# Performance work log

Hardware: AMD Instinct MI355X
Metric: run time of the kernel (lower is better)

The kernel has to match this reference:

```python
import jax, jax.numpy as jnp
import numpy as np

HEADS = 8
GS = 16
C = 512
E = 512
SCALE = (E / HEADS) ** -0.5
PNAMES = ['sa_qkv_w','sa_qkv_b','sa_pa_w','sa_pa_b','sa_ln1_g','sa_ln1_b','sa_f1_w','sa_f1_b','sa_f2_w','sa_f2_b','sa_ln2_g','sa_ln2_b','sa_c1_w','sa_c1_b','sa_c2_w','sa_c2_b','sa_bn_g','sa_bn_b','ca_q_w','ca_q_b','ca_k_w','ca_k_b','ca_v_w','ca_v_b','ca_pa_w','ca_pa_b','p_q_w','p_q_b','p_k_w','p_k_b','p_v_w','p_v_b','p_pa_w','p_pa_b','p_ln_g','p_ln_b','p_lin_w','p_lin_b']


def _ln(x, g, b, eps=1e-5):
    m = x.mean(-1, keepdims=True)
    v = jnp.var(x, axis=-1, keepdims=True)
    return (x - m) / jnp.sqrt(v + eps) * g + b


def _conv1x1(x, w, b):
    return jnp.einsum('bchw,oc->bohw', x, w) + b[None, :, None, None]


def _up_ac(x, out=GS):
    # bilinear upsample, align_corners=True (nn.UpsamplingBilinear2d)
    H = x.shape[2]
    pos = jnp.arange(out) * (H - 1) / (out - 1)
    lo = jnp.floor(pos).astype(jnp.int32)
    hi = jnp.minimum(lo + 1, H - 1)
    w = (pos - lo).astype(x.dtype)
    xr = x[:, :, lo, :] * (1 - w)[None, None, :, None] + x[:, :, hi, :] * w[None, None, :, None]
    return xr[:, :, :, lo] * (1 - w) + xr[:, :, :, hi] * w


def _asri(x, p):
    # Sequence_ASRI: GAP tokens -> attention over the batch axis -> pixel-shuffle back
    B = x.shape[0]; ch = E // HEADS
    gap = x.mean((2, 3))                                             # [B,C]
    qkv = (gap @ p['sa_qkv_w'].T + p['sa_qkv_b']).reshape(B, 4, ch, HEADS).transpose(1, 3, 0, 2)  # [4,H,B,ch]
    q, k, v, skip = qkv[0], qkv[1], qkv[2], qkv[3]
    attn = jax.nn.softmax(jnp.einsum('hbc,hdc->hbd', q, k) * SCALE, -1)  # [H,B,B]
    o = jnp.einsum('hbd,hdc->hbc', attn, v)
    merge = lambda t: t.transpose(1, 2, 0).reshape(B, E)             # 'head b c -> b (c head)'
    a = merge(o) @ p['sa_pa_w'].T + p['sa_pa_b'] + merge(skip)
    h = jax.nn.relu(_ln(a, p['sa_ln1_g'], p['sa_ln1_b']) @ p['sa_f1_w'].T + p['sa_f1_b'])
    a = h @ p['sa_f2_w'].T + p['sa_f2_b'] + a
    s = _ln(a, p['sa_ln2_g'], p['sa_ln2_b']) @ p['sa_c1_w'].T + p['sa_c1_b']  # [B,C*16]
    s = _up_ac(s.reshape(B, C, 4, 4))                                 # pixel shuffle p1=p2=4 then bilinear to 16x16
    s = _conv1x1(s, p['sa_c2_w'], p['sa_c2_b'])
    # BatchNorm2d in eval mode (running_mean=0, running_var=1, eps=1e-5)
    s = s / np.float32(np.sqrt(1.0 + 1e-5)) * p['sa_bn_g'][None, :, None, None] + p['sa_bn_b'][None, :, None, None]
    return x + jax.nn.relu(s)


def _sscm(x1, x2, p):
    # Sequence_SSCM: GAP-token q/k over batch axis, full spatial v
    B = x1.shape[0]; ch = E // HEADS
    q = (x1.mean((2, 3)) @ p['ca_q_w'].T + p['ca_q_b']).reshape(B, ch, HEADS).transpose(2, 0, 1)  # [H,B,ch]
    k = (x2.mean((2, 3)) @ p['ca_k_w'].T + p['ca_k_b']).reshape(B, ch, HEADS).transpose(2, 0, 1)
    v = _conv1x1(x2, p['ca_v_w'], p['ca_v_b']).reshape(B, ch, HEADS, GS, GS).transpose(2, 0, 1, 3, 4).reshape(HEADS, B, ch * GS * GS)
    attn = jax.nn.softmax(jnp.einsum('hbc,hdc->hbd', q, k) * SCALE, -1)  # [H,B,B]
    o = jnp.einsum('hbd,hdm->hbm', attn, v)
    o = o.reshape(HEADS, B, ch, GS, GS).transpose(1, 2, 0, 3, 4).reshape(B, E, GS, GS)
    return jax.nn.relu(_conv1x1(o, p['ca_pa_w'], p['ca_pa_b']))


def _pixel(x1, x2, p):
    # Pixel_SSCM: pixel-wise cross-batch attention (no scale -- matches source)
    B = x1.shape[0]; ch = E // HEADS; N = GS * GS
    split = lambda t: t.reshape(B, ch, HEADS, N).transpose(2, 0, 3, 1)   # 'b (c head) h w -> head b (h w) c'
    q = split(_conv1x1(x1, p['p_q_w'], p['p_q_b']))                      # [H,B,N,ch]
    k = split(_conv1x1(x2, p['p_k_w'], p['p_k_b']))
    v = split(_conv1x1(x2, p['p_v_w'], p['p_v_b'])).reshape(HEADS, B * N, ch)
    attn = jax.nn.softmax(jnp.einsum('hbnc,hqmc->hbqnm', q, k), -1)      # [H,B,B,N,N]
    attn = attn.transpose(1, 0, 3, 2, 4).reshape(B, HEADS, N, B * N)     # 'head b q h w -> b head h (q w)'
    o = jnp.einsum('bhnm,hmc->bhnc', attn, v)
    o = o.transpose(0, 3, 1, 2).reshape(B, E, GS, GS)                    # 'b head (h w) c -> b (c head) h w'
    o = _conv1x1(o, p['p_pa_w'], p['p_pa_b']) + x1
    t = o.reshape(B, C, N).transpose(0, 2, 1)                            # [B,N,C]
    t = jax.nn.relu(_ln(t, p['p_ln_g'], p['p_ln_b']) @ p['p_lin_w'].T + p['p_lin_b'])
    return t.transpose(0, 2, 1).reshape(B, C, GS, GS)


def _hrlm(p, xs, xq):
    sa_s = _asri(xs, p)
    sa_q = _asri(xq, p)
    ca_s = _sscm(sa_s, sa_q, p)
    ca_q = _sscm(sa_q, sa_s, p)
    return _pixel(sa_s, ca_q, p), _pixel(sa_q, ca_s, p)


def setup_inputs():
    key = jax.random.key(0)
    ks = iter(jax.random.split(key, 64))
    w = lambda *s: (jax.random.normal(next(ks), s) * 0.02).astype(jnp.float32)
    z = lambda n: jnp.zeros((n,), jnp.float32)
    o = lambda n: jnp.ones((n,), jnp.float32)
    return dict(
        fea_support=jax.random.normal(next(ks), (8, C, GS, GS), jnp.float32),
        fea_query=jax.random.normal(next(ks), (8, C, GS, GS), jnp.float32),
        sa_qkv_w=w(4 * E, C), sa_qkv_b=z(4 * E),
        sa_pa_w=w(E, E), sa_pa_b=z(E),
        sa_ln1_g=o(E), sa_ln1_b=z(E),
        sa_f1_w=w(E, E), sa_f1_b=z(E), sa_f2_w=w(E, E), sa_f2_b=z(E),
        sa_ln2_g=o(E), sa_ln2_b=z(E),
        sa_c1_w=w(C * 16, E), sa_c1_b=z(C * 16),
        sa_c2_w=w(C, E), sa_c2_b=z(C),
        sa_bn_g=o(C), sa_bn_b=z(C),
        ca_q_w=w(E, C), ca_q_b=z(E), ca_k_w=w(E, C), ca_k_b=z(E),
        ca_v_w=w(E, C), ca_v_b=z(E), ca_pa_w=w(C, E), ca_pa_b=z(C),
        p_q_w=w(E, C), p_q_b=z(E), p_k_w=w(E, C), p_k_b=z(E),
        p_v_w=w(E, C), p_v_b=z(E), p_pa_w=w(C, E), p_pa_b=z(C),
        p_ln_g=o(C), p_ln_b=z(C), p_lin_w=w(C, C), p_lin_b=z(C),
    )


def reference(fea_support, fea_query, sa_qkv_w, sa_qkv_b, sa_pa_w, sa_pa_b, sa_ln1_g, sa_ln1_b, sa_f1_w, sa_f1_b, sa_f2_w, sa_f2_b, sa_ln2_g, sa_ln2_b, sa_c1_w, sa_c1_b, sa_c2_w, sa_c2_b, sa_bn_g, sa_bn_b, ca_q_w, ca_q_b, ca_k_w, ca_k_b, ca_v_w, ca_v_b, ca_pa_w, ca_pa_b, p_q_w, p_q_b, p_k_w, p_k_b, p_v_w, p_v_b, p_pa_w, p_pa_b, p_ln_g, p_ln_b, p_lin_w, p_lin_b):
    p = dict(zip(PNAMES, (sa_qkv_w, sa_qkv_b, sa_pa_w, sa_pa_b, sa_ln1_g, sa_ln1_b, sa_f1_w, sa_f1_b, sa_f2_w, sa_f2_b, sa_ln2_g, sa_ln2_b, sa_c1_w, sa_c1_b, sa_c2_w, sa_c2_b, sa_bn_g, sa_bn_b, ca_q_w, ca_q_b, ca_k_w, ca_k_b, ca_v_w, ca_v_b, ca_pa_w, ca_pa_b, p_q_w, p_q_b, p_k_w, p_k_b, p_v_w, p_v_b, p_pa_w, p_pa_b, p_ln_g, p_ln_b, p_lin_w, p_lin_b)))
    return _hrlm(p, fea_support, fea_query)
```

## Files before the change

### kernel.cpp

```cpp
#include <hip/hip_runtime.h>
#include <cmath>

#define IMG 131072
#define BIGF 1048576

#define CF_RELU  1
#define CF_RES   2
#define CF_BN    4
#define CF_SPLIT 8
#define CF_TRANS 16

typedef __attribute__((ext_vector_type(8))) short short8;
typedef __attribute__((ext_vector_type(4))) short short4v;
typedef __attribute__((ext_vector_type(4))) float f32x4;

__device__ __forceinline__ float wave_sum(float v){
    #pragma unroll
    for (int off = 32; off; off >>= 1) v += __shfl_xor(v, off);
    return v;
}

__device__ __forceinline__ unsigned short bf16_rn(float x){
    union { float f; unsigned u; } v; v.f = x;
    unsigned r = v.u + 0x7FFF + ((v.u >> 16) & 1);
    return (unsigned short)(r >> 16);
}
__device__ __forceinline__ float bf16_to_f(unsigned short h){
    union { float f; unsigned u; } v; v.u = ((unsigned)h) << 16;
    return v.f;
}
__device__ __forceinline__ unsigned pk_hi(unsigned a, unsigned b){
    return __builtin_amdgcn_perm(b, a, 0x05040100u);
}
__device__ __forceinline__ unsigned pk_lo(unsigned a, unsigned b){
    return __builtin_amdgcn_perm(b, a, 0x07060302u);
}

struct GapJobs  { const float* x[2]; float* o[2]; };
struct G8Job    { const float* in; const float* W; const float* bias; const float* add; float* out; };
struct G8Jobs   { G8Job j[4]; };
struct AAJobs   { const float* qkv[2]; float* om[2]; };
struct LnJobs   { const float* in[2]; float* out[2]; };
struct UpJobs   { const float* in[2]; float* out[2]; };
struct SAJobs   { const float* q8[2]; const float* k8[2]; float* aw[2]; };
struct SPJobs   { const float* aw[2]; const float* v[2]; float* out[2]; };
struct ZJobs    { float* p[2]; };
struct ConvJob  { const float* X; const float* W; const float* B; const float* R;
                  const float* bng; const float* bnb; float* O; int flags; };
struct ConvJobs { ConvJob j[6]; };
struct PixJob   { const unsigned* Q; const unsigned* K; const unsigned* V; float* O; };
struct PixJobs  { PixJob j[2]; };

__global__ __launch_bounds__(64) void k_gap(GapJobs jo){
    const int br = blockIdx.y;
    const int bc = blockIdx.x;
    const int lane = threadIdx.x;
    const float* p = jo.x[br] + (size_t)bc * 256;
    float s = p[lane] + p[lane + 64] + p[lane + 128] + p[lane + 192];
    s = wave_sum(s);
    if (lane == 0) jo.o[br][bc] = s * (1.0f / 256.0f);
}

__global__ __launch_bounds__(64) void k_gemm8(G8Jobs jo, int add_off, int add_stride, int O, int relu){
    const G8Job j = jo.j[blockIdx.y];
    const int o = blockIdx.x;
    const int lane = threadIdx.x;
    const float* wr = j.W + (size_t)o * 512;
    float acc[8] = {0,0,0,0,0,0,0,0};
    #pragma unroll
    for (int i = 0; i < 8; i++){
        float w = wr[lane + 64*i];
        #pragma unroll
        for (int b = 0; b < 8; b++) acc[b] += w * j.in[b*512 + lane + 64*i];
    }
    #pragma unroll
    for (int b = 0; b < 8; b++) acc[b] = wave_sum(acc[b]);
    if (lane < 8){
        float v = acc[0];
        #pragma unroll
        for (int b = 1; b < 8; b++) if (lane == b) v = acc[b];
        v += j.bias[o];
        if (j.add) v += j.add[lane*add_stride + add_off + o];
        if (relu) v = fmaxf(v, 0.f);
        j.out[(size_t)lane * O + o] = v;
    }
}

__global__ __launch_bounds__(64) void k_asri_attn(AAJobs jo){
    const int br = blockIdx.y;
    const float* qkv = jo.qkv[br];
    const int h = blockIdx.x >> 3, b = blockIdx.x & 7, c = threadIdx.x;
    const int ci = c*8 + h;
    float qc = qkv[b*2048 + ci];
    float s[8];
    #pragma unroll
    for (int d = 0; d < 8; d++){
        float p = qc * qkv[d*2048 + 512 + ci];
        p = wave_sum(p);
        s[d] = p * 0.125f;
    }
    float m = s[0];
    #pragma unroll
    for (int d = 1; d < 8; d++) m = fmaxf(m, s[d]);
    float sum = 0.f;
    #pragma unroll
    for (int d = 0; d < 8; d++){ s[d] = __expf(s[d]-m); sum += s[d]; }
    float r = 1.f / sum;
    float oc = 0.f;
    #pragma unroll
    for (int d = 0; d < 8; d++) oc += s[d]*r * qkv[d*2048 + 1024 + ci];
    jo.om[br][b*512 + ci] = oc;
}

__global__ __launch_bounds__(64) void k_ln8(LnJobs jo,
    const float* __restrict__ g, const float* __restrict__ be)
{
    const int br = blockIdx.y;
    const int b = blockIdx.x, lane = threadIdx.x;
    const float* in = jo.in[br];
    float v[8]; float s = 0.f;
    #pragma unroll
    for (int i = 0; i < 8; i++){ v[i] = in[b*512 + lane + 64*i]; s += v[i]; }
    s = wave_sum(s);
    float mean = s * (1.f/512.f);
    float q = 0.f;
    #pragma unroll
    for (int i = 0; i < 8; i++){ float d = v[i]-mean; q += d*d; }
    q = wave_sum(q);
    float rstd = rsqrtf(q*(1.f/512.f) + 1e-5f);
    #pragma unroll
    for (int i = 0; i < 8; i++){
        int c = lane + 64*i;
        jo.out[br][b*512 + c] = (v[i]-mean)*rstd*g[c] + be[c];
    }
}

__global__ __launch_bounds__(256) void k_up(UpJobs jo){
    const int br = blockIdx.y;
    const int idx = blockIdx.x*256 + threadIdx.x;
    const int x = idx & 15, y = (idx >> 4) & 15, bc = idx >> 8;
    float px = (float)(x*3) / 15.0f, py = (float)(y*3) / 15.0f;
    int lx = (int)px, ly = (int)py;
    float wx = px - lx, wy = py - ly;
    int hx = min(lx+1, 3), hy = min(ly+1, 3);
    const float* p = jo.in[br] + (size_t)bc * 16;
    float v00 = p[ly*4+lx], v01 = p[ly*4+hx], v10 = p[hy*4+lx], v11 = p[hy*4+hx];
    float a0 = v00*(1.f-wy) + v10*wy;
    float a1 = v01*(1.f-wy) + v11*wy;
    jo.out[br][idx] = a0*(1.f-wx) + a1*wx;
}

__global__ __launch_bounds__(256) void k_zero(ZJobs jo){
    jo.p[blockIdx.y][(size_t)blockIdx.x*256 + threadIdx.x] = 0.f;
}

#define LDK 40
__device__ __forceinline__ void convm_body(
    const float* __restrict__ Xb, const float* __restrict__ W,
    const float* __restrict__ bias, const float* __restrict__ resb,
    const float* __restrict__ bng, const float* __restrict__ bnb, float bninv,
    float* __restrict__ outb, int flags, int o0, int n0, unsigned short* lds)
{
    const int tid512 = threadIdx.x;
    const int g   = tid512 >> 8;
    const int tid = tid512 & 255;
    unsigned short* sAh = lds + g*10240;
    unsigned short* sAl = sAh + 2560;
    unsigned short* sBh = sAl + 2560;
    unsigned short* sBl = sBh + 2560;
    const int wv = tid >> 6, lane = tid & 63;
    const int quad = lane >> 4, l16 = lane & 15;
    const int wo = (wv >> 1) * 32, wn = (wv & 1) * 32;
    const int so  = tid >> 2, sk8 = (tid & 3) * 8;
    const int sp  = tid & 15, sn  = (tid >> 4) * 4;

    const float* wrow = W + (size_t)(o0 + so)*512 + g*256 + sk8;
    const float* xrow = Xb + (size_t)(g*256 + 2*sp)*256 + n0 + sn;

    f32x4 acc[2][2] = {};
    float4 a0 = *(const float4*)(wrow);
    float4 a1 = *(const float4*)(wrow + 4);
    float4 x0 = *(const float4*)(xrow);
    float4 x1 = *(const float4*)(xrow + 256);

    for (int k0 = 0; k0 < 256; k0 += 32){
        __syncthreads();
        {
            float wa[8] = {a0.x,a0.y,a0.z,a0.w,a1.x,a1.y,a1.z,a1.w};
            #pragma unroll
            for (int j = 0; j < 4; j++){
                unsigned short h0 = bf16_rn(wa[2*j]);
                unsigned short h1 = bf16_rn(wa[2*j+1]);
                unsigned short g0 = bf16_rn(wa[2*j]   - bf16_to_f(h0));
                unsigned short g1 = bf16_rn(wa[2*j+1] - bf16_to_f(h1));
                *(unsigned*)&sAh[so*LDK + sk8 + 2*j] = (unsigned)h0 | ((unsigned)h1 << 16);
                *(unsigned*)&sAl[so*LDK + sk8 + 2*j] = (unsigned)g0 | ((unsigned)g1 << 16);
            }
            float xe[4] = {x0.x,x0.y,x0.z,x0.w};
            float xo[4] = {x1.x,x1.y,x1.z,x1.w};
            #pragma unroll
            for (int j = 0; j < 4; j++){
                unsigned short h0 = bf16_rn(xe[j]);
                unsigned short h1 = bf16_rn(xo[j]);
                unsigned short g0 = bf16_rn(xe[j] - bf16_to_f(h0));
                unsigned short g1 = bf16_rn(xo[j] - bf16_to_f(h1));
                *(unsigned*)&sBh[(sn+j)*LDK + 2*sp] = (unsigned)h0 | ((unsigned)h1 << 16);
                *(unsigned*)&sBl[(sn+j)*LDK + 2*sp] = (unsigned)g0 | ((unsigned)g1 << 16);
            }
        }
        __syncthreads();
        if (k0 + 32 < 256){
            a0 = *(const float4*)(wrow + k0 + 32);
            a1 = *(const float4*)(wrow + k0 + 36);
            x0 = *(const float4*)(xrow + (size_t)(k0+32)*256);
            x1 = *(const float4*)(xrow + (size_t)(k0+32)*256 + 256);
        }
        short8 ah[2], al[2], bh[2], bl[2];
        #pragma unroll
        for (int t = 0; t < 2; t++){
            int ai = (wo + 16*t + l16)*LDK + quad*8;
            ah[t] = *(const short8*)&sAh[ai];
            al[t] = *(const short8*)&sAl[ai];
            int bi = (wn + 16*t + l16)*LDK + quad*8;
            bh[t] = *(const short8*)&sBh[bi];
            bl[t] = *(const short8*)&sBl[bi];
        }
        #pragma unroll
        for (int mt = 0; mt < 2; mt++){
            #pragma unroll
            for (int nt = 0; nt < 2; nt++){
                acc[mt][nt] = __builtin_amdgcn_mfma_f32_16x16x32_bf16(ah[mt], bh[nt], acc[mt][nt], 0, 0, 0);
                acc[mt][nt] = __builtin_amdgcn_mfma_f32_16x16x32_bf16(ah[mt], bl[nt], acc[mt][nt], 0, 0, 0);
                acc[mt][nt] = __builtin_amdgcn_mfma_f32_16x16x32_bf16(al[mt], bh[nt], acc[mt][nt], 0, 0, 0);
            }
        }
    }
    __syncthreads();
    float* red = (float*)lds;
    if (g == 1){
        float* r = red + tid*20;
        #pragma unroll
        for (int mt = 0; mt < 2; mt++)
            #pragma unroll
            for (int nt = 0; nt < 2; nt++)
                *(f32x4*)(r + (mt*2+nt)*4) = acc[mt][nt];
    }
    __syncthreads();
    if (g == 0){
        float* r = red + tid*20;
        #pragma unroll
        for (int mt = 0; mt < 2; mt++)
            #pragma unroll
            for (int nt = 0; nt < 2; nt++){
                f32x4 o4 = *(const f32x4*)(r + (mt*2+nt)*4);
                acc[mt][nt] += o4;
            }
        #pragma unroll
        for (int mt = 0; mt < 2; mt++){
            #pragma unroll
            for (int nt = 0; nt < 2; nt++){
                const int n  = n0 + wn + 16*nt + l16;
                const int ob = o0 + wo + 16*mt + quad*4;
                #pragma unroll
                for (int rr = 0; rr < 4; rr++){
                    const int o = ob + rr;
                    float v = acc[mt][nt][rr] + bias[o];
                    if (flags & CF_BN)   v = v*(bninv*bng[o]) + bnb[o];
                    if (flags & CF_RELU) v = fmaxf(v, 0.f);
                    if (flags & CF_RES)  v += resb[(size_t)o*256 + n];
                    if (flags & CF_SPLIT){
                        unsigned short hi = bf16_rn(v);
                        unsigned short lo = bf16_rn(v - bf16_to_f(hi));
                        unsigned pk = (unsigned)hi | ((unsigned)lo << 16);
                        unsigned* op = (unsigned*)outb;
                        if (flags & CF_TRANS) op[(size_t)n*512 + (o&7)*64 + (o>>3)] = pk;
                        else                  op[(size_t)o*256 + n] = pk;
                    } else {
                        outb[(size_t)o*256 + n] = v;
                    }
                }
            }
        }
    }
}

__global__ __launch_bounds__(512) void k_convm(ConvJobs jo, float bninv)
{
    __shared__ unsigned short lds[20480];
    const int z = blockIdx.z;
    const ConvJob j = jo.j[z >> 3];
    const int b = z & 7;
    convm_body(j.X + (size_t)b*IMG, j.W, j.B, j.R ? j.R + (size_t)b*IMG : nullptr,
               j.bng, j.bnb, bninv, j.O + (size_t)b*IMG, j.flags,
               blockIdx.y*64, blockIdx.x*64, lds);
}

__global__ __launch_bounds__(64) void k_sscm_attn(SAJobs jo)
{
    const int br = blockIdx.y;
    const int h = blockIdx.x >> 3, b = blockIdx.x & 7, c = threadIdx.x;
    const int ci = c*8 + h;
    float qc = jo.q8[br][b*512 + ci];
    float s[8];
    #pragma unroll
    for (int d = 0; d < 8; d++){
        float p = qc * jo.k8[br][d*512 + ci];
        p = wave_sum(p);
        s[d] = p * 0.125f;
    }
    float m = s[0];
    #pragma unroll
    for (int d = 1; d < 8; d++) m = fmaxf(m, s[d]);
    float sum = 0.f;
    #pragma unroll
    for (int d = 0; d < 8; d++){ s[d] = __expf(s[d]-m); sum += s[d]; }
    float r = 1.f/sum;
    if (c < 8){
        float v = s[0];
        #pragma unroll
        for (int d = 1; d < 8; d++) if (c == d) v = s[d];
        jo.aw[br][blockIdx.x*8 + c] = v*r;
    }
}

__global__ __launch_bounds__(256) void k_sscm_apply(SPJobs jo)
{
    const int br = blockIdx.y;
    const int idx = blockIdx.x*256 + threadIdx.x;
    const int pix = idx & 255, e = (idx >> 8) & 511, b = idx >> 17;
    const int h = e & 7;
    const float* aw = jo.aw[br] + (h*8 + b)*8;
    const float* v = jo.v[br];
    float acc = 0.f;
    #pragma unroll
    for (int d = 0; d < 8; d++) acc += aw[d] * v[(size_t)d*IMG + (size_t)e*256 + pix];
    jo.out[br][idx] = acc;
}

__global__ __launch_bounds__(256) void k_pixel_mfma(PixJobs jo)
{
    __shared__ char smem[61440];
    unsigned short* sQh = (unsigned short*)smem;
    unsigned short* sQl = sQh + 2*64*40;
    unsigned short* sKh = sQl + 2*64*40;
    unsigned short* sKl = sKh + 2*128*40;
    unsigned short* sP  = (unsigned short*)smem;
    unsigned short* sVh = sP  + 4*64*40;
    unsigned short* sVl = sVh + 4*64*40;

    const int br = blockIdx.y >> 3, b = blockIdx.y & 7;
    const PixJob J = jo.j[br];
    const int nt = blockIdx.x & 3, d = blockIdx.x >> 2;
    const int h = blockIdx.z;
    const int tid = threadIdx.x;
    const int wv = tid >> 6, lane = tid & 63;
    const int quad = lane >> 4, l16 = lane & 15;
    const int n0 = nt * 64;

    {
        const unsigned* Qt = J.Q + (size_t)b*IMG + (size_t)n0*512 + h*64;
        const int q = tid >> 2, i0 = (tid & 3) * 16;
        const unsigned* src = Qt + (size_t)q*512 + i0;
        uint4 w0 = *(const uint4*)(src);
        uint4 w1 = *(const uint4*)(src + 4);
        uint4 w2 = *(const uint4*)(src + 8);
        uint4 w3 = *(const uint4*)(src + 12);
        unsigned hb[8], lb[8];
        hb[0]=pk_hi(w0.x,w0.y); hb[1]=pk_hi(w0.z,w0.w); hb[2]=pk_hi(w1.x,w1.y); hb[3]=pk_hi(w1.z,w1.w);
        hb[4]=pk_hi(w2.x,w2.y); hb[5]=pk_hi(w2.z,w2.w); hb[6]=pk_hi(w3.x,w3.y); hb[7]=pk_hi(w3.z,w3.w);
        lb[0]=pk_lo(w0.x,w0.y); lb[1]=pk_lo(w0.z,w0.w); lb[2]=pk_lo(w1.x,w1.y); lb[3]=pk_lo(w1.z,w1.w);
        lb[4]=pk_lo(w2.x,w2.y); lb[5]=pk_lo(w2.z,w2.w); lb[6]=pk_lo(w3.x,w3.y); lb[7]=pk_lo(w3.z,w3.w);
        int dst = (i0>>5)*2560 + q*40 + (i0&31);
        *(uint4*)&sQh[dst]     = *(uint4*)&hb[0];
        *(uint4*)&sQh[dst + 8] = *(uint4*)&hb[4];
        *(uint4*)&sQl[dst]     = *(uint4*)&lb[0];
        *(uint4*)&sQl[dst + 8] = *(uint4*)&lb[4];
    }
    __syncthreads();

    short8 bqh[2], bql[2];
    #pragma unroll
    for (int ks = 0; ks < 2; ks++){
        int idx = ks*2560 + (wv*16 + l16)*40 + quad*8;
        bqh[ks] = *(const short8*)&sQh[idx];
        bql[ks] = *(const short8*)&sQl[idx];
    }

    f32x4 S[16] = {};
    #pragma unroll
    for (int hm = 0; hm < 2; hm++){
        __syncthreads();
        {
            const unsigned* Kt = J.K + (size_t)d*IMG + (size_t)hm*128*512 + h*64;
            const int mloc = tid & 127, cb0 = tid >> 7;
            #pragma unroll
            for (int p = 0; p < 4; p++){
                int cb = cb0 + 2*p;
                const unsigned* src = Kt + (size_t)mloc*512 + cb*8;
                uint4 wa = *(const uint4*)(src);
                uint4 wb = *(const uint4*)(src + 4);
                union { short8 s; unsigned u[4]; } hu, lu;
                hu.u[0]=pk_hi(wa.x,wa.y); hu.u[1]=pk_hi(wa.z,wa.w);
                hu.u[2]=pk_hi(wb.x,wb.y); hu.u[3]=pk_hi(wb.z,wb.w);
                lu.u[0]=pk_lo(wa.x,wa.y); lu.u[1]=pk_lo(wa.z,wa.w);
                lu.u[2]=pk_lo(wb.x,wb.y); lu.u[3]=pk_lo(wb.z,wb.w);
                int idx = (cb>>2)*5120 + mloc*40 + (cb&3)*8;
                *(short8*)&sKh[idx] = hu.s;
                *(short8*)&sKl[idx] = lu.s;
            }
        }
        __syncthreads();
        #pragma unroll
        for (int mtl = 0; mtl < 8; mtl++){
            #pragma unroll
            for (int ks = 0; ks < 2; ks++){
                int idx = ks*5120 + (mtl*16 + l16)*40 + quad*8;
                short8 ah = *(const short8*)&sKh[idx];
                short8 al = *(const short8*)&sKl[idx];
                S[hm*8+mtl] = __builtin_amdgcn_mfma_f32_16x16x32_bf16(ah, bqh[ks], S[hm*8+mtl], 0, 0, 0);
                S[hm*8+mtl] = __builtin_amdgcn_mfma_f32_16x16x32_bf16(ah, bql[ks], S[hm*8+mtl], 0, 0, 0);
                S[hm*8+mtl] = __builtin_amdgcn_mfma_f32_16x16x32_bf16(al, bqh[ks], S[hm*8+mtl], 0, 0, 0);
            }
        }
    }

    {
        float mx = -3.4e38f;
        #pragma unroll
        for (int t = 0; t < 16; t++)
            #pragma unroll
            for (int r = 0; r < 4; r++) mx = fmaxf(mx, S[t][r]);
        mx = fmaxf(mx, __shfl_xor(mx, 16));
        mx = fmaxf(mx, __shfl_xor(mx, 32));
        float sum = 0.f;
        #pragma unroll
        for (int t = 0; t < 16; t++)
            #pragma unroll
            for (int r = 0; r < 4; r++){ S[t][r] = __expf(S[t][r]-mx); sum += S[t][r]; }
        sum += __shfl_xor(sum, 16);
        sum += __shfl_xor(sum, 32);
        float rr = 1.f/sum;
        #pragma unroll
        for (int t = 0; t < 16; t++)
            #pragma unroll
            for (int r = 0; r < 4; r++) S[t][r] *= rr;
    }

    f32x4 oac[4] = {};
    #pragma unroll
    for (int hm = 0; hm < 2; hm++){
        __syncthreads();
        #pragma unroll
        for (int mtl = 0; mtl < 8; mtl++){
            short4v p4;
            #pragma unroll
            for (int r = 0; r < 4; r++) p4[r] = (short)bf16_rn(S[hm*8+mtl][r]);
            int idx = (mtl>>1)*2560 + (wv*16 + l16)*40 + 16*(mtl&1) + quad*4;
            *(short4v*)&sP[idx] = p4;
        }
        {
            const unsigned* Vp = J.V + (size_t)d*IMG + (size_t)h*256 + hm*128;
            const int mp = tid & 63, c0 = tid >> 6;
            #pragma unroll
            for (int p = 0; p < 16; p++){
                int c = c0 + 4*p;
                const unsigned* src = Vp + (size_t)c*2048 + 2*mp;
                uint2 w = *(const uint2*)(src);
                int idx = (mp>>4)*2560 + c*40 + ((2*mp)&31);
                *(unsigned*)&sVh[idx] = pk_hi(w.x, w.y);
                *(unsigned*)&sVl[idx] = pk_lo(w.x, w.y);
            }
        }
        __syncthreads();
        #pragma unroll
        for (int ks = 0; ks < 4; ks++){
            int pidx = ks*2560 + (wv*16 + l16)*40 + quad*8;
            short8 bp = *(const short8*)&sP[pidx];
            #pragma unroll
            for (int ct = 0; ct < 4; ct++){
                int vidx = ks*2560 + (ct*16 + l16)*40 + quad*8;
                short8 vh = *(const short8*)&sVh[vidx];
                short8 vl = *(const short8*)&sVl[vidx];
                oac[ct] = __builtin_amdgcn_mfma_f32_16x16x32_bf16(vh, bp, oac[ct], 0, 0, 0);
                oac[ct] = __builtin_amdgcn_mfma_f32_16x16x32_bf16(vl, bp, oac[ct], 0, 0, 0);
            }
        }
    }

    {
        float* Ob = J.O + (size_t)b * IMG;
        const int q = n0 + wv*16 + l16;
        #pragma unroll
        for (int ct = 0; ct < 4; ct++){
            #pragma unroll
            for (int r = 0; r < 4; r++){
                int c = ct*16 + quad*4 + r;
                unsafeAtomicAdd(&Ob[(size_t)(c*8+h)*256 + q], oac[ct][r]);
            }
        }
    }
}

__global__ __launch_bounds__(64) void k_ln_pix(LnJobs jo,
    const float* __restrict__ g, const float* __restrict__ be)
{
    const int br = blockIdx.y;
    const int bn = blockIdx.x;
    const int b = bn >> 8, n = bn & 255;
    const int lane = threadIdx.x;
    const float* p = jo.in[br] + (size_t)b*IMG + n;
    float v[8]; float s = 0.f;
    #pragma unroll
    for (int i = 0; i < 8; i++){ v[i] = p[(size_t)(lane + 64*i)*256]; s += v[i]; }
    s = wave_sum(s);
    float mean = s * (1.f/512.f);
    float q = 0.f;
    #pragma unroll
    for (int i = 0; i < 8; i++){ float d = v[i]-mean; q += d*d; }
    q = wave_sum(q);
    float rstd = rsqrtf(q*(1.f/512.f) + 1e-5f);
    #pragma unroll
    for (int i = 0; i < 8; i++){
        int c = lane + 64*i;
        jo.out[br][(size_t)b*IMG + (size_t)c*256 + n] = (v[i]-mean)*rstd*g[c] + be[c];
    }
}

extern "C" void kernel_launch(void* const* d_in, const int* in_sizes, int n_in,
                              void* d_out, int out_size, void* d_ws, size_t ws_size,
                              hipStream_t stream)
{
    const float* xs    = (const float*)d_in[0];
    const float* xq    = (const float*)d_in[1];
    const float* qkvw  = (const float*)d_in[2];  const float* qkvb = (const float*)d_in[3];
    const float* paw   = (const float*)d_in[4];  const float* pab  = (const float*)d_in[5];
    const float* ln1g  = (const float*)d_in[6];  const float* ln1b = (const float*)d_in[7];
    const float* f1w   = (const float*)d_in[8];  const float* f1b  = (const float*)d_in[9];
    const float* f2w   = (const float*)d_in[10]; const float* f2b  = (const float*)d_in[11];
    const float* ln2g  = (const float*)d_in[12]; const float* ln2b = (const float*)d_in[13];
    const float* c1w   = (const float*)d_in[14]; const float* c1b  = (const float*)d_in[15];
    const float* c2w   = (const float*)d_in[16]; const float* c2b  = (const float*)d_in[17];
    const float* bng   = (const float*)d_in[18]; const float* bnb  = (const float*)d_in[19];
    const float* caqw  = (const float*)d_in[20]; const float* caqb = (const float*)d_in[21];
    const float* cakw  = (const float*)d_in[22]; const float* cakb = (const float*)d_in[23];
    const float* cavw  = (const float*)d_in[24]; const float* cavb = (const float*)d_in[25];
    const float* capw  = (const float*)d_in[26]; const float* capb = (const float*)d_in[27];
    const float* pqw   = (const float*)d_in[28]; const float* pqb  = (const float*)d_in[29];
    const float* pkw   = (const float*)d_in[30]; const float* pkb  = (const float*)d_in[31];
    const float* pvw   = (const float*)d_in[32]; const float* pvb  = (const float*)d_in[33];
    const float* ppw   = (const float*)d_in[34]; const float* ppb  = (const float*)d_in[35];
    const float* plng  = (const float*)d_in[36]; const float* plnb = (const float*)d_in[37];
    const float* plinw = (const float*)d_in[38]; const float* plinb= (const float*)d_in[39];

    const size_t SMF = 262144;
    float* ws = (float*)d_ws;
    float* smb = ws;
    float* B[12];
    for (int i = 0; i < 12; i++) B[i] = ws + SMF + (size_t)i*BIGF;
    float* sa_s = B[0]; float* sa_q = B[1];
    float* ca_s = B[2]; float* ca_q = B[3];
    const bool paired_pixel = ws_size >= (SMF + 12*(size_t)BIGF)*sizeof(float) + 1024;

    auto SM = [&](int br){ return smb + (size_t)br*131072; };
    auto GAP=[&](int br){ return SM(br); };            auto QKV=[&](int br){ return SM(br)+4096; };
    auto OM =[&](int br){ return SM(br)+20480; };      auto AA =[&](int br){ return SM(br)+24576; };
    auto HB =[&](int br){ return SM(br)+28672; };      auto A2 =[&](int br){ return SM(br)+32768; };
    auto LNB=[&](int br){ return SM(br)+36864; };      auto S8 =[&](int br){ return SM(br)+40960; };
    auto ATW=[&](int br){ return SM(br)+106496; };     auto Q8 =[&](int br){ return SM(br)+107008; };
    auto K8 =[&](int br){ return SM(br)+111104; };

    const float bninv = 1.0f / sqrtf(1.0f + 1e-5f);
    float* out0 = (float*)d_out;
    float* out1 = out0 + (size_t)BIGF;

    {
        GapJobs gj = {{xs, xq}, {GAP(0), GAP(1)}};
        k_gap<<<dim3(4096,2), 64, 0, stream>>>(gj);
        G8Jobs qj = {{{GAP(0), qkvw, qkvb, nullptr, QKV(0)}, {GAP(1), qkvw, qkvb, nullptr, QKV(1)}}};
        k_gemm8<<<dim3(2048,2), 64, 0, stream>>>(qj, 0, 0, 2048, 0);
        AAJobs aj = {{QKV(0), QKV(1)}, {OM(0), OM(1)}};
        k_asri_attn<<<dim3(64,2), 64, 0, stream>>>(aj);
        G8Jobs pj = {{{OM(0), paw, pab, QKV(0), AA(0)}, {OM(1), paw, pab, QKV(1), AA(1)}}};
        k_gemm8<<<dim3(512,2), 64, 0, stream>>>(pj, 1536, 2048, 512, 0);
        LnJobs l1 = {{AA(0), AA(1)}, {LNB(0), LNB(1)}};
        k_ln8<<<dim3(8,2), 64, 0, stream>>>(l1, ln1g, ln1b);
        G8Jobs fj = {{{LNB(0), f1w, f1b, nullptr, HB(0)}, {LNB(1), f1w, f1b, nullptr, HB(1)}}};
        k_gemm8<<<dim3(512,2), 64, 0, stream>>>(fj, 0, 0, 512, 1);
        G8Jobs f2j = {{{HB(0), f2w, f2b, AA(0), A2(0)}, {HB(1), f2w, f2b, AA(1), A2(1)}}};
        k_gemm8<<<dim3(512,2), 64, 0, stream>>>(f2j, 0, 512, 512, 0);
        LnJobs l2 = {{A2(0), A2(1)}, {LNB(0), LNB(1)}};
        k_ln8<<<dim3(8,2), 64, 0, stream>>>(l2, ln2g, ln2b);
        G8Jobs cj = {{{LNB(0), c1w, c1b, nullptr, S8(0)}, {LNB(1), c1w, c1b, nullptr, S8(1)}}};
        k_gemm8<<<dim3(8192,2), 64, 0, stream>>>(cj, 0, 0, 8192, 0);
        UpJobs uj = {{S8(0), S8(1)}, {B[4], B[5]}};
        k_up<<<dim3(4096,2), 256, 0, stream>>>(uj);
        ConvJobs c2j = {};
        c2j.j[0] = {B[4], c2w, c2b, xs, bng, bnb, sa_s, CF_BN|CF_RELU|CF_RES};
        c2j.j[1] = {B[5], c2w, c2b, xq, bng, bnb, sa_q, CF_BN|CF_RELU|CF_RES};
        k_convm<<<dim3(4,8,16), 512, 0, stream>>>(c2j, bninv);
    }

    {
        GapJobs gj = {{sa_s, sa_q}, {GAP(0), GAP(1)}};
        k_gap<<<dim3(4096,2), 64, 0, stream>>>(gj);
        G8Jobs qj = {{{GAP(0), caqw, caqb, nullptr, Q8(0)},
                      {GAP(1), cakw, cakb, nullptr, K8(0)},
                      {GAP(1), caqw, caqb, nullptr, Q8(1)},
                      {GAP(0), cakw, cakb, nullptr, K8(1)}}};
        k_gemm8<<<dim3(512,4), 64, 0, stream>>>(qj, 0, 0, 512, 0);
        SAJobs sj = {{Q8(0), Q8(1)}, {K8(0), K8(1)}, {ATW(0), ATW(1)}};
        k_sscm_attn<<<dim3(64,2), 64, 0, stream>>>(sj);
        ConvJobs vj = {};
        vj.j[0] = {sa_q, cavw, cavb, nullptr, nullptr, nullptr, B[4], 0};
        vj.j[1] = {sa_s, cavw, cavb, nullptr, nullptr, nullptr, B[5], 0};
        k_convm<<<dim3(4,8,16), 512, 0, stream>>>(vj, 1.f);
        SPJobs pj = {{ATW(0), ATW(1)}, {B[4], B[5]}, {B[6], B[7]}};
        k_sscm_apply<<<dim3(4096,2), 256, 0, stream>>>(pj);
        ConvJobs aj = {};
        aj.j[0] = {B[6], capw, capb, nullptr, nullptr, nullptr, ca_s, CF_RELU};
        aj.j[1] = {B[7], capw, capb, nullptr, nullptr, nullptr, ca_q, CF_RELU};
        k_convm<<<dim3(4,8,16), 512, 0, stream>>>(aj, 1.f);
    }

    if (paired_pixel){
        ConvJobs qkvj = {};
        qkvj.j[0] = {sa_s, pqw, pqb, nullptr, nullptr, nullptr, B[4],  CF_SPLIT|CF_TRANS};
        qkvj.j[1] = {ca_q, pkw, pkb, nullptr, nullptr, nullptr, B[5],  CF_SPLIT|CF_TRANS};
        qkvj.j[2] = {ca_q, pvw, pvb, nullptr, nullptr, nullptr, B[6],  CF_SPLIT};
        qkvj.j[3] = {sa_q, pqw, pqb, nullptr, nullptr, nullptr, B[8],  CF_SPLIT|CF_TRANS};
        qkvj.j[4] = {ca_s, pkw, pkb, nullptr, nullptr, nullptr, B[9],  CF_SPLIT|CF_TRANS};
        qkvj.j[5] = {ca_s, pvw, pvb, nullptr, nullptr, nullptr, B[10], CF_SPLIT};
        k_convm<<<dim3(4,8,48), 512, 0, stream>>>(qkvj, 1.f);
        ZJobs zj = {{B[7], B[11]}};
        k_zero<<<dim3(4096,2), 256, 0, stream>>>(zj);
        PixJobs pxj = {{{(const unsigned*)B[4], (const unsigned*)B[5], (const unsigned*)B[6], B[7]},
                        {(const unsigned*)B[8], (const unsigned*)B[9], (const unsigned*)B[10], B[11]}}};
        k_pixel_mfma<<<dim3(32,16,8), 256, 0, stream>>>(pxj);
        ConvJobs ppj = {};
        ppj.j[0] = {B[7],  ppw, ppb, sa_s, nullptr, nullptr, out0, CF_RES};
        ppj.j[1] = {B[11], ppw, ppb, sa_q, nullptr, nullptr, out1, CF_RES};
        k_convm<<<dim3(4,8,16), 512, 0, stream>>>(ppj, 1.f);
        LnJobs lj = {{out0, out1}, {B[4], B[8]}};
        k_ln_pix<<<dim3(2048,2), 64, 0, stream>>>(lj, plng, plnb);
        ConvJobs lnj = {};
        lnj.j[0] = {B[4], plinw, plinb, nullptr, nullptr, nullptr, out0, CF_RELU};
        lnj.j[1] = {B[8], plinw, plinb, nullptr, nullptr, nullptr, out1, CF_RELU};
        k_convm<<<dim3(4,8,16), 512, 0, stream>>>(lnj, 1.f);
    } else {
        auto pixel1 = [&](const float* x1, const float* x2, float* out){
            ConvJobs qkvj = {};
            qkvj.j[0] = {x1, pqw, pqb, nullptr, nullptr, nullptr, B[4], CF_SPLIT|CF_TRANS};
            qkvj.j[1] = {x2, pkw, pkb, nullptr, nullptr, nullptr, B[5], CF_SPLIT|CF_TRANS};
            qkvj.j[2] = {x2, pvw, pvb, nullptr, nullptr, nullptr, B[6], CF_SPLIT};
            k_convm<<<dim3(4,8,24), 512, 0, stream>>>(qkvj, 1.f);
            ZJobs zj = {{B[7], B[7]}};
            k_zero<<<dim3(4096,1), 256, 0, stream>>>(zj);
            PixJobs pxj = {{{(const unsigned*)B[4], (const unsigned*)B[5], (const unsigned*)B[6], B[7]},
                            {(const unsigned*)B[4], (const unsigned*)B[5], (const unsigned*)B[6], B[7]}}};
            k_pixel_mfma<<<dim3(32,8,8), 256, 0, stream>>>(pxj);
            ConvJobs ppj = {};
            ppj.j[0] = {B[7], ppw, ppb, x1, nullptr, nullptr, out, CF_RES};
            k_convm<<<dim3(4,8,8), 512, 0, stream>>>(ppj, 1.f);
            LnJobs lj = {{out, out}, {B[4], B[4]}};
            k_ln_pix<<<dim3(2048,1), 64, 0, stream>>>(lj, plng, plnb);
            ConvJobs lnj = {};
            lnj.j[0] = {B[4], plinw, plinb, nullptr, nullptr, nullptr, out, CF_RELU};
            k_convm<<<dim3(4,8,8), 512, 0, stream>>>(lnj, 1.f);
        };
        pixel1(sa_s, ca_q, out0);
        pixel1(sa_q, ca_s, out1);
    }

    (void)in_sizes; (void)n_in; (void)out_size;
}
```

Measured before the change: 492.6 us.

## Shrink pixel-attention LDS footprint and coalesce transposed split conv output

The pixel attention kernel now stages K and V in smaller 64-row chunks over more loop iterations, cutting shared memory per block from 60KB to 40KB so more blocks can be resident per CU. The cost is extra barriers and a finer load/compute interleave. Separately, the conv kernel's transposed split-output path permutes the weight rows and swaps the MFMA operand order. This lets each lane write contiguous positions in the transposed output instead of doing strided scatter stores.

```diff
diff --git a/kernel.cpp b/kernel.cpp
--- a/kernel.cpp
+++ b/kernel.cpp
@@ -174,7 +174,11 @@
     const int so  = tid >> 2, sk8 = (tid & 3) * 8;
     const int sp  = tid & 15, sn  = (tid >> 4) * 4;
 
-    const float* wrow = W + (size_t)(o0 + so)*512 + g*256 + sk8;
+    const bool trans = (flags & CF_TRANS) != 0;
+    int so_g = o0 + so;
+    if (trans) so_g = ((so_g & 63) << 3) | (so_g >> 6);
+
+    const float* wrow = W + (size_t)so_g*512 + g*256 + sk8;
     const float* xrow = Xb + (size_t)(g*256 + 2*sp)*256 + n0 + sn;
 
     f32x4 acc[2][2] = {};
@@ -225,13 +229,25 @@
             bh[t] = *(const short8*)&sBh[bi];
             bl[t] = *(const short8*)&sBl[bi];
         }
-        #pragma unroll
-        for (int mt = 0; mt < 2; mt++){
-            #pragma unroll
-            for (int nt = 0; nt < 2; nt++){
-                acc[mt][nt] = __builtin_amdgcn_mfma_f32_16x16x32_bf16(ah[mt], bh[nt], acc[mt][nt], 0, 0, 0);
-                acc[mt][nt] = __builtin_amdgcn_mfma_f32_16x16x32_bf16(ah[mt], bl[nt], acc[mt][nt], 0, 0, 0);
-                acc[mt][nt] = __builtin_amdgcn_mfma_f32_16x16x32_bf16(al[mt], bh[nt], acc[mt][nt], 0, 0, 0);
+        if (trans){
+            #pragma unroll
+            for (int mt = 0; mt < 2; mt++){
+                #pragma unroll
+                for (int nt = 0; nt < 2; nt++){
+                    acc[mt][nt] = __builtin_amdgcn_mfma_f32_16x16x32_bf16(bh[nt], ah[mt], acc[mt][nt], 0, 0, 0);
+                    acc[mt][nt] = __builtin_amdgcn_mfma_f32_16x16x32_bf16(bl[nt], ah[mt], acc[mt][nt], 0, 0, 0);
+                    acc[mt][nt] = __builtin_amdgcn_mfma_f32_16x16x32_bf16(bh[nt], al[mt], acc[mt][nt], 0, 0, 0);
+                }
+            }
+        } else {
+            #pragma unroll
+            for (int mt = 0; mt < 2; mt++){
+                #pragma unroll
+                for (int nt = 0; nt < 2; nt++){
+                    acc[mt][nt] = __builtin_amdgcn_mfma_f32_16x16x32_bf16(ah[mt], bh[nt], acc[mt][nt], 0, 0, 0);
+                    acc[mt][nt] = __builtin_amdgcn_mfma_f32_16x16x32_bf16(ah[mt], bl[nt], acc[mt][nt], 0, 0, 0);
+                    acc[mt][nt] = __builtin_amdgcn_mfma_f32_16x16x32_bf16(al[mt], bh[nt], acc[mt][nt], 0, 0, 0);
+                }
             }
         }
     }
@@ -255,28 +271,47 @@
                 f32x4 o4 = *(const f32x4*)(r + (mt*2+nt)*4);
                 acc[mt][nt] += o4;
             }
-        #pragma unroll
-        for (int mt = 0; mt < 2; mt++){
-            #pragma unroll
-            for (int nt = 0; nt < 2; nt++){
-                const int n  = n0 + wn + 16*nt + l16;
-                const int ob = o0 + wo + 16*mt + quad*4;
+        if (trans){
+            unsigned* op = (unsigned*)outb;
+            #pragma unroll
+            for (int mt = 0; mt < 2; mt++){
                 #pragma unroll
-                for (int rr = 0; rr < 4; rr++){
-                    const int o = ob + rr;
-                    float v = acc[mt][nt][rr] + bias[o];
-                    if (flags & CF_BN)   v = v*(bninv*bng[o]) + bnb[o];
-                    if (flags & CF_RELU) v = fmaxf(v, 0.f);
-                    if (flags & CF_RES)  v += resb[(size_t)o*256 + n];
-                    if (flags & CF_SPLIT){
+                for (int nt = 0; nt < 2; nt++){
+                    const int p  = o0 + wo + 16*mt + l16;
+                    const int nb = n0 + wn + 16*nt + quad*4;
+                    const int osrc = ((p & 63) << 3) | (p >> 6);
+                    const float bs = bias[osrc];
+                    #pragma unroll
+                    for (int rr = 0; rr < 4; rr++){
+                        float v = acc[mt][nt][rr] + bs;
                         unsigned short hi = bf16_rn(v);
                         unsigned short lo = bf16_rn(v - bf16_to_f(hi));
-                        unsigned pk = (unsigned)hi | ((unsigned)lo << 16);
-                        unsigned* op = (unsigned*)outb;
-                        if (flags & CF_TRANS) op[(size_t)n*512 + (o&7)*64 + (o>>3)] = pk;
-                        else                  op[(size_t)o*256 + n] = pk;
-                    } else {
-                        outb[(size_t)o*256 + n] = v;
+                        op[(size_t)(nb+rr)*512 + p] = (unsigned)hi | ((unsigned)lo << 16);
+                    }
+                }
+            }
+        } else {
+            #pragma unroll
+            for (int mt = 0; mt < 2; mt++){
+                #pragma unroll
+                for (int nt = 0; nt < 2; nt++){
+                    const int n  = n0 + wn + 16*nt + l16;
+                    const int ob = o0 + wo + 16*mt + quad*4;
+                    #pragma unroll
+                    for (int rr = 0; rr < 4; rr++){
+                        const int o = ob + rr;
+                        float v = acc[mt][nt][rr] + bias[o];
+                        if (flags & CF_BN)   v = v*(bninv*bng[o]) + bnb[o];
+                        if (flags & CF_RELU) v = fmaxf(v, 0.f);
+                        if (flags & CF_RES)  v += resb[(size_t)o*256 + n];
+                        if (flags & CF_SPLIT){
+                            unsigned short hi = bf16_rn(v);
+                            unsigned short lo = bf16_rn(v - bf16_to_f(hi));
+                            unsigned pk = (unsigned)hi | ((unsigned)lo << 16);
+                            ((unsigned*)outb)[(size_t)o*256 + n] = pk;
+                        } else {
+                            outb[(size_t)o*256 + n] = v;
+                        }
                     }
                 }
             }
@@ -339,14 +374,14 @@
 
 __global__ __launch_bounds__(256) void k_pixel_mfma(PixJobs jo)
 {
-    __shared__ char smem[61440];
+    __shared__ char smem[40960];
     unsigned short* sQh = (unsigned short*)smem;
     unsigned short* sQl = sQh + 2*64*40;
     unsigned short* sKh = sQl + 2*64*40;
-    unsigned short* sKl = sKh + 2*128*40;
+    unsigned short* sKl = sKh + 2*64*40;
     unsigned short* sP  = (unsigned short*)smem;
-    unsigned short* sVh = sP  + 4*64*40;
-    unsigned short* sVl = sVh + 4*64*40;
+    unsigned short* sVh = sKh;
+    unsigned short* sVl = sKl;
 
     const int br = blockIdx.y >> 3, b = blockIdx.y & 7;
     const PixJob J = jo.j[br];
@@ -388,14 +423,14 @@
 
     f32x4 S[16] = {};
     #pragma unroll
-    for (int hm = 0; hm < 2; hm++){
-        __syncthreads();
+    for (int mq = 0; mq < 4; mq++){
+        if (mq) __syncthreads();
         {
-            const unsigned* Kt = J.K + (size_t)d*IMG + (size_t)hm*128*512 + h*64;
-            const int mloc = tid & 127, cb0 = tid >> 7;
-            #pragma unroll
-            for (int p = 0; p < 4; p++){
-                int cb = cb0 + 2*p;
+            const unsigned* Kt = J.K + (size_t)d*IMG + (size_t)(mq*64)*512 + h*64;
+            const int mloc = tid & 63, cb0 = tid >> 6;
+            #pragma unroll
+            for (int p = 0; p < 2; p++){
+                int cb = cb0 + 4*p;
                 const unsigned* src = Kt + (size_t)mloc*512 + cb*8;
                 uint4 wa = *(const uint4*)(src);
                 uint4 wb = *(const uint4*)(src + 4);
@@ -404,22 +439,23 @@
                 hu.u[2]=pk_hi(wb.x,wb.y); hu.u[3]=pk_hi(wb.z,wb.w);
                 lu.u[0]=pk_lo(wa.x,wa.y); lu.u[1]=pk_lo(wa.z,wa.w);
                 lu.u[2]=pk_lo(wb.x,wb.y); lu.u[3]=pk_lo(wb.z,wb.w);
-                int idx = (cb>>2)*5120 + mloc*40 + (cb&3)*8;
+                int idx = (cb>>2)*2560 + mloc*40 + (cb&3)*8;
                 *(short8*)&sKh[idx] = hu.s;
                 *(short8*)&sKl[idx] = lu.s;
             }
         }
         __syncthreads();
         #pragma unroll
-        for (int mtl = 0; mtl < 8; mtl++){
+        for (int mtl = 0; mtl < 4; mtl++){
+            int t = mq*4 + mtl;
             #pragma unroll
             for (int ks = 0; ks < 2; ks++){
-                int idx = ks*5120 + (mtl*16 + l16)*40 + quad*8;
+                int idx = ks*2560 + (mtl*16 + l16)*40 + quad*8;
                 short8 ah = *(const short8*)&sKh[idx];
                 short8 al = *(const short8*)&sKl[idx];
-                S[hm*8+mtl] = __builtin_amdgcn_mfma_f32_16x16x32_bf16(ah, bqh[ks], S[hm*8+mtl], 0, 0, 0);
-                S[hm*8+mtl] = __builtin_amdgcn_mfma_f32_16x16x32_bf16(ah, bql[ks], S[hm*8+mtl], 0, 0, 0);
-                S[hm*8+mtl] = __builtin_amdgcn_mfma_f32_16x16x32_bf16(al, bqh[ks], S[hm*8+mtl], 0, 0, 0);
+                S[t] = __builtin_amdgcn_mfma_f32_16x16x32_bf16(ah, bqh[ks], S[t], 0, 0, 0);
+                S[t] = __builtin_amdgcn_mfma_f32_16x16x32_bf16(ah, bql[ks], S[t], 0, 0, 0);
+                S[t] = __builtin_amdgcn_mfma_f32_16x16x32_bf16(al, bqh[ks], S[t], 0, 0, 0);
             }
         }
     }
@@ -452,37 +488,43 @@
         __syncthreads();
         #pragma unroll
         for (int mtl = 0; mtl < 8; mtl++){
+            int t = hm*8 + mtl;
             short4v p4;
             #pragma unroll
-            for (int r = 0; r < 4; r++) p4[r] = (short)bf16_rn(S[hm*8+mtl][r]);
+            for (int r = 0; r < 4; r++) p4[r] = (short)bf16_rn(S[t][r]);
             int idx = (mtl>>1)*2560 + (wv*16 + l16)*40 + 16*(mtl&1) + quad*4;
             *(short4v*)&sP[idx] = p4;
         }
-        {
-            const unsigned* Vp = J.V + (size_t)d*IMG + (size_t)h*256 + hm*128;
-            const int mp = tid & 63, c0 = tid >> 6;
-            #pragma unroll
-            for (int p = 0; p < 16; p++){
-                int c = c0 + 4*p;
-                const unsigned* src = Vp + (size_t)c*2048 + 2*mp;
-                uint2 w = *(const uint2*)(src);
-                int idx = (mp>>4)*2560 + c*40 + ((2*mp)&31);
-                *(unsigned*)&sVh[idx] = pk_hi(w.x, w.y);
-                *(unsigned*)&sVl[idx] = pk_lo(w.x, w.y);
-            }
-        }
-        __syncthreads();
-        #pragma unroll
-        for (int ks = 0; ks < 4; ks++){
-            int pidx = ks*2560 + (wv*16 + l16)*40 + quad*8;
-            short8 bp = *(const short8*)&sP[pidx];
-            #pragma unroll
-            for (int ct = 0; ct < 4; ct++){
-                int vidx = ks*2560 + (ct*16 + l16)*40 + quad*8;
-                short8 vh = *(const short8*)&sVh[vidx];
-                short8 vl = *(const short8*)&sVl[vidx];
-                oac[ct] = __builtin_amdgcn_mfma_f32_16x16x32_bf16(vh, bp, oac[ct], 0, 0, 0);
-                oac[ct] = __builtin_amdgcn_mfma_f32_16x16x32_bf16(vl, bp, oac[ct], 0, 0, 0);
+        #pragma unroll
+        for (int sub = 0; sub < 2; sub++){
+            if (sub) __syncthreads();
+            {
+                const unsigned* Vp = J.V + (size_t)d*IMG + (size_t)h*256 + hm*128 + sub*64;
+                const int mp = tid & 31, c0 = tid >> 5;
+                #pragma unroll
+                for (int p = 0; p < 8; p++){
+                    int c = c0 + 8*p;
+                    const unsigned* src = Vp + (size_t)c*2048 + 2*mp;
+                    uint2 w = *(const uint2*)(src);
+                    int idx = ((2*mp)>>5)*2560 + c*40 + ((2*mp)&31);
+                    *(unsigned*)&sVh[idx] = pk_hi(w.x, w.y);
+                    *(unsigned*)&sVl[idx] = pk_lo(w.x, w.y);
+                }
+            }
+            __syncthreads();
+            #pragma unroll
+            for (int l = 0; l < 2; l++){
+                int gks = sub*2 + l;
+                int pidx = gks*2560 + (wv*16 + l16)*40 + quad*8;
+                short8 bp = *(const short8*)&sP[pidx];
+                #pragma unroll
+                for (int ct = 0; ct < 4; ct++){
+                    int vidx = l*2560 + (ct*16 + l16)*40 + quad*8;
+                    short8 vh = *(const short8*)&sVh[vidx];
+                    short8 vl = *(const short8*)&sVl[vidx];
+                    oac[ct] = __builtin_amdgcn_mfma_f32_16x16x32_bf16(vh, bp, oac[ct], 0, 0, 0);
+                    oac[ct] = __builtin_amdgcn_mfma_f32_16x16x32_bf16(vl, bp, oac[ct], 0, 0, 0);
+                }
             }
         }
     }
```

After: 473.6 us. -3.9%, faster.
